# Optimization experiments

Measured on AMD Instinct MI355X. Metric: run time of the kernel, lower is better.

Reference implementation:

```python
import jax, jax.numpy as jnp
import numpy as np

N, E, IN, H, D = 50000, 800000, 256, 4, 32
ALPHA = 0.2


def setup_inputs() -> dict:
    key = jax.random.key(0)
    ks = jax.random.split(key, 8)
    return {
        "node_feature": jax.random.normal(ks[0], (N, IN), dtype=jnp.float32),
        "edge_feature": jax.random.normal(ks[1], (E, IN), dtype=jnp.float32),
        "src": jax.random.randint(ks[2], (E,), 0, N, dtype=jnp.int32),
        "dst": jax.random.randint(ks[3], (E,), 0, N, dtype=jnp.int32),
        "W": jax.random.normal(ks[4], (IN, H * D), dtype=jnp.float32) * (1.0 / np.sqrt(IN)),
        "attn_l": jax.random.normal(ks[5], (H, D), dtype=jnp.float32),
        "attn_r": jax.random.normal(ks[6], (H, D), dtype=jnp.float32),
        "attn_e": jax.random.normal(ks[7], (H, D), dtype=jnp.float32),
    }


def reference(node_feature, edge_feature, src, dst, W, attn_l, attn_r, attn_e):
    n = node_feature.shape[0]
    h, d = attn_l.shape
    # shared linear projection for node and edge features (feat_drop is identity, p=0)
    ft = (node_feature @ W).reshape(n, h, d)            # [N,H,D]
    e_ft = (edge_feature @ W).reshape(-1, h, d)          # [E,H,D]
    # per-head scalar attention logits
    a1 = jnp.einsum("nhd,hd->nh", ft, attn_l)            # [N,H]
    a2 = jnp.einsum("nhd,hd->nh", ft, attn_r)            # [N,H]
    a3 = jnp.einsum("ehd,hd->eh", e_ft, attn_e)          # [E,H]
    logits = jax.nn.leaky_relu(a1[src] + a3 + a2[dst], negative_slope=ALPHA)  # [E,H]
    # edge softmax grouped by destination node
    m = jax.ops.segment_max(logits, dst, num_segments=n)  # [N,H]
    ex = jnp.exp(logits - m[dst])                        # [E,H]
    s = jax.ops.segment_sum(ex, dst, num_segments=n)     # [N,H]
    a = ex / s[dst]                                       # [E,H] (attn_drop identity)
    # weighted messages: attention-weighted src feats + attention-weighted edge feats
    aw = a[:, :, None]                                    # [E,H,1]
    f_cat = e_ft * aw + ft[src] * aw                      # [E,H,D]
    node_out = jax.ops.segment_sum(f_cat, dst, num_segments=n)  # [N,H,D]
    ret1 = jax.nn.elu(node_out.reshape(n, h * d))
    ret2 = jax.nn.elu(f_cat.reshape(-1, h * d))
    return ret1, ret2
```

## Files before the change

### kernel.cpp

```cpp
#include <hip/hip_runtime.h>
#include <hip/hip_bf16.h>
#include <math.h>

#define NN    50000
#define EE    800000
#define IN_F  256
#define HH    4
#define DD    32
#define OUT_F 128
#define ALPHA 0.2f

typedef float f32x4 __attribute__((ext_vector_type(4)));
typedef short bf16x8 __attribute__((ext_vector_type(8)));

__device__ __forceinline__ float elu_f(float x) { return x > 0.0f ? x : expm1f(x); }

__device__ __forceinline__ unsigned short f2bf(float x) {
    union { float f; unsigned u; } v; v.f = x;
    unsigned r = (v.u + 0x7FFFu + ((v.u >> 16) & 1u)) >> 16;
    return (unsigned short)r;
}
__device__ __forceinline__ float bf2f(unsigned short h) {
    union { unsigned u; float f; } v; v.u = ((unsigned)h) << 16; return v.f;
}

__global__ __launch_bounds__(256) void k_prepw(const float* __restrict__ W,
        unsigned short* __restrict__ Whp, unsigned short* __restrict__ Wlp) {
    int i = blockIdx.x * 256 + threadIdx.x;
    int j = i & 7, lane = (i >> 3) & 63, cf = (i >> 9) & 7, t = i >> 12;
    int krow = 32 * t + 8 * (lane >> 4) + j;
    int col  = 16 * cf + (lane & 15);
    float x = W[krow * OUT_F + col];
    unsigned short h = f2bf(x);
    unsigned short lo = f2bf(x - bf2f(h));
    Whp[i] = h; Wlp[i] = lo;
}

template <int MODE, bool EFB>
__global__ __launch_bounds__(256, 4) void k_gemm(const float* __restrict__ X, int M,
        const unsigned short* __restrict__ Whp, const unsigned short* __restrict__ Wlp,
        const float* __restrict__ av0, const float* __restrict__ av1,
        const int* __restrict__ src, const int* __restrict__ dst,
        const float* __restrict__ a1, const float* __restrict__ a2,
        float* __restrict__ Yf, unsigned short* __restrict__ Yh,
        float* __restrict__ o1, float* __restrict__ o2,
        float* __restrict__ ssum) {
    __shared__ unsigned short Asw[2][2][64 * 64];
    __shared__ float p_lds[4][64];
    __shared__ float q_lds[4][64];

    const int tid = threadIdx.x;
    const int w = tid >> 6;
    const int l = tid & 63;
    const int base = blockIdx.x * 64;

    const int srow = tid >> 2;
    const int scg  = tid & 3;
    int gr = base + srow; if (gr > M - 1) gr = M - 1;
    const float* xp = X + (size_t)gr * IN_F + scg * 16;

    float4 xs[4];
    #pragma unroll
    for (int q = 0; q < 4; ++q) xs[q] = *(const float4*)(xp + q * 4);

    auto cvtwrite = [&](int buf) {
        unsigned short h[16], lo[16];
        const float* xf = (const float*)xs;
        #pragma unroll
        for (int k = 0; k < 16; ++k) {
            h[k]  = f2bf(xf[k]);
            lo[k] = f2bf(xf[k] - bf2f(h[k]));
        }
        const unsigned sw = (unsigned)((srow & 7) << 4);
        const unsigned b0 = (unsigned)(srow * 128 + scg * 32) ^ sw;
        const unsigned b1 = (unsigned)(srow * 128 + scg * 32 + 16) ^ sw;
        char* ph = (char*)&Asw[buf][0][0];
        char* pl = (char*)&Asw[buf][1][0];
        *(bf16x8*)(ph + b0) = *(const bf16x8*)(h);
        *(bf16x8*)(ph + b1) = *(const bf16x8*)(h + 8);
        *(bf16x8*)(pl + b0) = *(const bf16x8*)(lo);
        *(bf16x8*)(pl + b1) = *(const bf16x8*)(lo + 8);
    };
    cvtwrite(0);

    f32x4 acc[4][2];
    #pragma unroll
    for (int rf = 0; rf < 4; ++rf)
        #pragma unroll
        for (int cf = 0; cf < 2; ++cf)
            acc[rf][cf] = (f32x4){0.f, 0.f, 0.f, 0.f};

    #pragma unroll
    for (int c = 0; c < 4; ++c) {
        __syncthreads();
        if (c < 3) {
            #pragma unroll
            for (int q = 0; q < 4; ++q)
                xs[q] = *(const float4*)(xp + (c + 1) * 64 + q * 4);
        }
        bf16x8 Bh[2][2], Bl[2][2];
        #pragma unroll
        for (int ks = 0; ks < 2; ++ks)
            #pragma unroll
            for (int cf = 0; cf < 2; ++cf) {
                size_t off = ((size_t)((c * 2 + ks) * 8 + (w * 2 + cf)) * 64 + l) * 8;
                Bh[ks][cf] = *(const bf16x8*)(Whp + off);
                Bl[ks][cf] = *(const bf16x8*)(Wlp + off);
            }
        const char* ph = (const char*)&Asw[c & 1][0][0];
        const char* pl = (const char*)&Asw[c & 1][1][0];
        #pragma unroll
        for (int rf = 0; rf < 4; ++rf) {
            const int row = rf * 16 + (l & 15);
            const unsigned sw = (unsigned)((row & 7) << 4);
            #pragma unroll
            for (int ks = 0; ks < 2; ++ks) {
                const unsigned ba = (unsigned)(row * 128 + ks * 64 + (l >> 4) * 16) ^ sw;
                bf16x8 ah = *(const bf16x8*)(ph + ba);
                bf16x8 al = *(const bf16x8*)(pl + ba);
                #pragma unroll
                for (int cf = 0; cf < 2; ++cf) {
                    acc[rf][cf] = __builtin_amdgcn_mfma_f32_16x16x32_bf16(ah, Bh[ks][cf], acc[rf][cf], 0, 0, 0);
                    acc[rf][cf] = __builtin_amdgcn_mfma_f32_16x16x32_bf16(al, Bh[ks][cf], acc[rf][cf], 0, 0, 0);
                    acc[rf][cf] = __builtin_amdgcn_mfma_f32_16x16x32_bf16(ah, Bl[ks][cf], acc[rf][cf], 0, 0, 0);
                }
            }
        }
        if (c < 3) cvtwrite((c + 1) & 1);
    }

    #pragma unroll
    for (int rf = 0; rf < 4; ++rf)
        #pragma unroll
        for (int cf = 0; cf < 2; ++cf)
            #pragma unroll
            for (int r = 0; r < 4; ++r) {
                int grow = base + rf * 16 + (l >> 4) * 4 + r;
                size_t oidx = (size_t)grow * OUT_F + w * 32 + cf * 16 + (l & 15);
                if (MODE == 0) {
                    if (grow < M) Yf[oidx] = acc[rf][cf][r];
                } else if (EFB) {
                    Yh[oidx] = f2bf(acc[rf][cf][r]);
                } else {
                    Yf[oidx] = acc[rf][cf][r];
                }
            }

    const float b0 = av0[w * DD + (l & 15)];
    const float b1 = av0[w * DD + 16 + (l & 15)];
    float c0v = 0.f, c1v = 0.f;
    if (MODE == 0) { c0v = av1[w * DD + (l & 15)]; c1v = av1[w * DD + 16 + (l & 15)]; }

    float pv[4][4], qv[4][4];
    #pragma unroll
    for (int rf = 0; rf < 4; ++rf)
        #pragma unroll
        for (int r = 0; r < 4; ++r) {
            pv[rf][r] = acc[rf][0][r] * b0 + acc[rf][1][r] * b1;
            if (MODE == 0) qv[rf][r] = acc[rf][0][r] * c0v + acc[rf][1][r] * c1v;
        }
    #pragma unroll
    for (int o = 1; o <= 8; o <<= 1)
        #pragma unroll
        for (int rf = 0; rf < 4; ++rf)
            #pragma unroll
            for (int r = 0; r < 4; ++r) {
                pv[rf][r] += __shfl_xor(pv[rf][r], o);
                if (MODE == 0) qv[rf][r] += __shfl_xor(qv[rf][r], o);
            }
    if ((l & 15) == 0) {
        const int hi = l >> 4;
        #pragma unroll
        for (int rf = 0; rf < 4; ++rf)
            #pragma unroll
            for (int r = 0; r < 4; ++r) {
                p_lds[w][rf * 16 + hi * 4 + r] = pv[rf][r];
                if (MODE == 0) q_lds[w][rf * 16 + hi * 4 + r] = qv[rf][r];
            }
    }
    __syncthreads();

    const int grow = base + l;
    if (MODE == 0) {
        if (grow < M) {
            o1[(size_t)grow * HH + w] = p_lds[w][l];
            o2[(size_t)grow * HH + w] = q_lds[w][l];
        }
    } else {
        const int s = src[grow], t2 = dst[grow];
        float lg = p_lds[w][l] + a1[(size_t)s * HH + w] + a2[(size_t)t2 * HH + w];
        lg = fmaxf(lg, ALPHA * lg);
        float exv = expf(lg);
        o1[(size_t)grow * HH + w] = exv;
        atomicAdd(&ssum[t2 * HH + w], exv);
    }
}

__global__ __launch_bounds__(256) void k_hist(const int* __restrict__ dst,
        int* __restrict__ hist) {
    int i = blockIdx.x * 256 + threadIdx.x;
    if (i < EE) atomicAdd(&hist[dst[i]], 1);
}

__global__ __launch_bounds__(1024) void k_scan(const int* __restrict__ hist,
        int* __restrict__ rowptr, int* __restrict__ cursor) {
    __shared__ int part[1024];
    const int t = threadIdx.x;
    const int CH = (NN + 1023) / 1024;
    const int b = t * CH;
    int s = 0;
    for (int i = 0; i < CH; ++i) {
        int idx = b + i;
        if (idx < NN) s += hist[idx];
    }
    part[t] = s;
    __syncthreads();
    int total = s;
    for (int o = 1; o < 1024; o <<= 1) {
        int u = (t >= o) ? part[t - o] : 0;
        __syncthreads();
        part[t] += u;
        __syncthreads();
    }
    int run = part[t] - total;
    for (int i = 0; i < CH; ++i) {
        int idx = b + i;
        if (idx < NN) {
            rowptr[idx] = run;
            cursor[idx] = run;
            run += hist[idx];
        }
    }
}

__global__ __launch_bounds__(256) void k_scatter(const int* __restrict__ dst,
        int* __restrict__ cursor, int* __restrict__ order) {
    int i = blockIdx.x * 256 + threadIdx.x;
    if (i < EE) {
        int pos = atomicAdd(&cursor[dst[i]], 1);
        order[pos] = i;
    }
}

template <bool EFB>
__global__ __launch_bounds__(256, 8) void k_agg2(const int* __restrict__ order,
        const int* __restrict__ src, const int* __restrict__ dst,
        const float* __restrict__ ft, const float* __restrict__ exq,
        const float* __restrict__ ssum, const unsigned short* __restrict__ eftb,
        float* __restrict__ ret2, float* __restrict__ node_out) {
    __shared__ int eL[64], sL[64], dL[64];
    __shared__ int sent[2];
    const int tid = threadIdx.x;
    const int base = blockIdx.x * 64;
    if (tid < 64) {
        int e = order[base + tid];
        eL[tid] = e;
        sL[tid] = src[e];
        dL[tid] = dst[e];
    } else if (tid == 64) {
        sent[0] = (blockIdx.x > 0) ? dst[order[base - 1]] : -1;
    } else if (tid == 65) {
        sent[1] = (base + 64 < EE) ? dst[order[base + 64]] : -1;
    }
    __syncthreads();

    const int w = tid >> 6, l = tid & 63;
    const int W0 = w * 16, W1 = W0 + 15;
    const int c0 = l * 2, h = l >> 4;

    const int dprev  = (W0 == 0)  ? sent[0] : dL[W0 - 1];
    const int dafter = (W1 == 63) ? sent[1] : dL[W1 + 1];

    float acc0 = 0.f, acc1 = 0.f;
    int dcur = dL[W0];
    bool touch_start = true;

    #pragma unroll 4
    for (int r = W0; r <= W1; ++r) {
        const int e = eL[r], s = sL[r], d = dL[r];
        if (d != dcur) {
            const size_t o = (size_t)dcur * OUT_F + c0;
            if (touch_start && dcur == dprev) {
                atomicAdd(&node_out[o], acc0);
                atomicAdd(&node_out[o + 1], acc1);
            } else {
                *(float2*)(node_out + o) = make_float2(acc0, acc1);
            }
            acc0 = acc1 = 0.f; dcur = d; touch_start = false;
        }
        const float a = exq[(size_t)e * HH + h] * __frcp_rn(ssum[d * HH + h]);
        float e0, e1;
        if (EFB) {
            ushort2 ev = *(const ushort2*)(eftb + (size_t)e * OUT_F + c0);
            e0 = bf2f(ev.x); e1 = bf2f(ev.y);
        } else {
            float2 ev = *(const float2*)(ret2 + (size_t)e * OUT_F + c0);
            e0 = ev.x; e1 = ev.y;
        }
        float2 fv = *(const float2*)(ft + (size_t)s * OUT_F + c0);
        float f0 = (e0 + fv.x) * a;
        float f1 = (e1 + fv.y) * a;
        acc0 += f0; acc1 += f1;
        *(float2*)(ret2 + (size_t)e * OUT_F + c0) = make_float2(elu_f(f0), elu_f(f1));
    }
    {
        const size_t o = (size_t)dcur * OUT_F + c0;
        const bool at = (touch_start && dcur == dprev) || (dcur == dafter);
        if (at) {
            atomicAdd(&node_out[o], acc0);
            atomicAdd(&node_out[o + 1], acc1);
        } else {
            *(float2*)(node_out + o) = make_float2(acc0, acc1);
        }
    }
}

__global__ __launch_bounds__(256) void k_elu1(const float4* __restrict__ node_out,
        float4* __restrict__ ret1) {
    const int i = blockIdx.x * blockDim.x + threadIdx.x;
    if (i < NN * OUT_F / 4) {
        float4 v = node_out[i];
        ret1[i] = make_float4(elu_f(v.x), elu_f(v.y), elu_f(v.z), elu_f(v.w));
    }
}

extern "C" void kernel_launch(void* const* d_in, const int* in_sizes, int n_in,
                              void* d_out, int out_size, void* d_ws, size_t ws_size,
                              hipStream_t stream) {
    const float* nf     = (const float*)d_in[0];
    const float* ef     = (const float*)d_in[1];
    const int*   src    = (const int*)d_in[2];
    const int*   dst    = (const int*)d_in[3];
    const float* W      = (const float*)d_in[4];
    const float* attn_l = (const float*)d_in[5];
    const float* attn_r = (const float*)d_in[6];
    const float* attn_e = (const float*)d_in[7];

    float* ret1 = (float*)d_out;
    float* ret2 = ret1 + (size_t)NN * OUT_F;

    char* wsp = (char*)d_ws;
    auto take = [&](size_t bytes) { char* p = wsp; wsp += (bytes + 511) & ~size_t(511); return p; };
    float* ft     = (float*)take((size_t)NN * OUT_F * 4);
    float* a1buf  = (float*)take((size_t)NN * HH * 4);
    float* a2buf  = (float*)take((size_t)NN * HH * 4);
    float* exq    = (float*)take((size_t)EE * HH * 4);
    float* ssum   = (float*)take((size_t)NN * HH * 4);
    unsigned short* Whp = (unsigned short*)take(32768 * 2);
    unsigned short* Wlp = (unsigned short*)take(32768 * 2);
    int* hist   = (int*)take((size_t)NN * 4);
    int* rowptr = (int*)take((size_t)NN * 4);
    int* cursor = (int*)take((size_t)NN * 4);
    int* order  = (int*)take((size_t)EE * 4);

    const size_t eft_bytes = (size_t)EE * OUT_F * 2;
    const size_t used = (size_t)(wsp - (char*)d_ws);
    const bool efb = (used + eft_bytes + 1024) <= ws_size;
    unsigned short* eftb = efb ? (unsigned short*)take(eft_bytes) : nullptr;

    hipMemsetAsync(ssum, 0, (size_t)NN * HH * 4, stream);
    hipMemsetAsync(hist, 0, (size_t)NN * 4, stream);
    hipMemsetAsync(ret1, 0, (size_t)NN * OUT_F * 4, stream);

    k_prepw<<<128, 256, 0, stream>>>(W, Whp, Wlp);
    k_hist<<<(EE + 255) / 256, 256, 0, stream>>>(dst, hist);
    k_scan<<<1, 1024, 0, stream>>>(hist, rowptr, cursor);
    k_scatter<<<(EE + 255) / 256, 256, 0, stream>>>(dst, cursor, order);

    k_gemm<0, false><<<(NN + 63) / 64, 256, 0, stream>>>(nf, NN, Whp, Wlp,
            attn_l, attn_r, nullptr, nullptr, nullptr, nullptr,
            ft, nullptr, a1buf, a2buf, nullptr);

    if (efb) {
        k_gemm<1, true><<<EE / 64, 256, 0, stream>>>(ef, EE, Whp, Wlp,
                attn_e, nullptr, src, dst, a1buf, a2buf,
                nullptr, eftb, exq, nullptr, ssum);
        k_agg2<true><<<EE / 64, 256, 0, stream>>>(order, src, dst, ft, exq,
                ssum, eftb, ret2, ret1);
    } else {
        k_gemm<1, false><<<EE / 64, 256, 0, stream>>>(ef, EE, Whp, Wlp,
                attn_e, nullptr, src, dst, a1buf, a2buf,
                ret2, nullptr, exq, nullptr, ssum);
        k_agg2<false><<<EE / 64, 256, 0, stream>>>(order, src, dst, ft, exq,
                ssum, nullptr, ret2, ret1);
    }
    k_elu1<<<(NN * OUT_F / 4 + 255) / 256, 256, 0, stream>>>(
            (const float4*)ret1, (float4*)ret1);
}
```

Measured before the change: 811.8 us.

## Store node projections in bf16, fuse setup kernels, prefetch edge gather indices

Node projection ft is now stored as bf16 instead of fp32, which halves the bytes of the random per-edge src gathers in the aggregation kernel. The W prep, dst histogram and zeroing of ssum and ret1 are merged into one setup kernel, replacing two memsets and two launches. In the edge GEMM, the src/dst indices and the a1/a2 logit gathers are issued before the MFMA loop so their latency overlaps compute. The fp32 fallback path is dropped, so the edge bf16 buffer is always taken from the workspace, and rounding ft to bf16 adds precision loss.

```diff
diff --git a/kernel.cpp b/kernel.cpp
--- a/kernel.cpp
+++ b/kernel.cpp
@@ -24,25 +24,43 @@
     union { unsigned u; float f; } v; v.u = ((unsigned)h) << 16; return v.f;
 }
 
-__global__ __launch_bounds__(256) void k_prepw(const float* __restrict__ W,
-        unsigned short* __restrict__ Whp, unsigned short* __restrict__ Wlp) {
-    int i = blockIdx.x * 256 + threadIdx.x;
-    int j = i & 7, lane = (i >> 3) & 63, cf = (i >> 9) & 7, t = i >> 12;
-    int krow = 32 * t + 8 * (lane >> 4) + j;
-    int col  = 16 * cf + (lane & 15);
-    float x = W[krow * OUT_F + col];
-    unsigned short h = f2bf(x);
-    unsigned short lo = f2bf(x - bf2f(h));
-    Whp[i] = h; Wlp[i] = lo;
-}
-
-template <int MODE, bool EFB>
+#define PREP_B 128
+#define HIST_B 3125
+#define SSUM_B 196
+#define RET1_B 6250
+__global__ __launch_bounds__(256) void k_setup(const float* __restrict__ W,
+        unsigned short* __restrict__ Whp, unsigned short* __restrict__ Wlp,
+        const int* __restrict__ dst, int* __restrict__ hist,
+        float4* __restrict__ ssum4, float4* __restrict__ ret14) {
+    const int b = blockIdx.x, tid = threadIdx.x;
+    if (b < PREP_B) {
+        int i = b * 256 + tid;
+        int j = i & 7, lane = (i >> 3) & 63, cf = (i >> 9) & 7, t = i >> 12;
+        int krow = 32 * t + 8 * (lane >> 4) + j;
+        int col  = 16 * cf + (lane & 15);
+        float x = W[krow * OUT_F + col];
+        unsigned short h = f2bf(x);
+        Whp[i] = h;
+        Wlp[i] = f2bf(x - bf2f(h));
+    } else if (b < PREP_B + HIST_B) {
+        int i = (b - PREP_B) * 256 + tid;
+        atomicAdd(&hist[dst[i]], 1);
+    } else if (b < PREP_B + HIST_B + SSUM_B) {
+        int i = (b - PREP_B - HIST_B) * 256 + tid;
+        if (i < NN * HH / 4) ssum4[i] = make_float4(0.f, 0.f, 0.f, 0.f);
+    } else {
+        int i = (b - PREP_B - HIST_B - SSUM_B) * 256 + tid;
+        ret14[i] = make_float4(0.f, 0.f, 0.f, 0.f);
+    }
+}
+
+template <int MODE>
 __global__ __launch_bounds__(256, 4) void k_gemm(const float* __restrict__ X, int M,
         const unsigned short* __restrict__ Whp, const unsigned short* __restrict__ Wlp,
         const float* __restrict__ av0, const float* __restrict__ av1,
         const int* __restrict__ src, const int* __restrict__ dst,
         const float* __restrict__ a1, const float* __restrict__ a2,
-        float* __restrict__ Yf, unsigned short* __restrict__ Yh,
+        unsigned short* __restrict__ Yh,
         float* __restrict__ o1, float* __restrict__ o2,
         float* __restrict__ ssum) {
     __shared__ unsigned short Asw[2][2][64 * 64];
@@ -53,6 +71,9 @@
     const int w = tid >> 6;
     const int l = tid & 63;
     const int base = blockIdx.x * 64;
+
+    int s_e = 0, t_e = 0;
+    if (MODE == 1) { s_e = src[base + l]; t_e = dst[base + l]; }
 
     const int srow = tid >> 2;
     const int scg  = tid & 3;
@@ -83,6 +104,12 @@
     };
     cvtwrite(0);
 
+    float a1v = 0.f, a2v = 0.f;
+    if (MODE == 1) {
+        a1v = a1[(size_t)s_e * HH + w];
+        a2v = a2[(size_t)t_e * HH + w];
+    }
+
     f32x4 acc[4][2];
     #pragma unroll
     for (int rf = 0; rf < 4; ++rf)
@@ -136,14 +163,9 @@
             #pragma unroll
             for (int r = 0; r < 4; ++r) {
                 int grow = base + rf * 16 + (l >> 4) * 4 + r;
-                size_t oidx = (size_t)grow * OUT_F + w * 32 + cf * 16 + (l & 15);
-                if (MODE == 0) {
-                    if (grow < M) Yf[oidx] = acc[rf][cf][r];
-                } else if (EFB) {
-                    Yh[oidx] = f2bf(acc[rf][cf][r]);
-                } else {
-                    Yf[oidx] = acc[rf][cf][r];
-                }
+                if (MODE == 1 || grow < M)
+                    Yh[(size_t)grow * OUT_F + w * 32 + cf * 16 + (l & 15)] =
+                        f2bf(acc[rf][cf][r]);
             }
 
     const float b0 = av0[w * DD + (l & 15)];
@@ -187,23 +209,16 @@
             o2[(size_t)grow * HH + w] = q_lds[w][l];
         }
     } else {
-        const int s = src[grow], t2 = dst[grow];
-        float lg = p_lds[w][l] + a1[(size_t)s * HH + w] + a2[(size_t)t2 * HH + w];
+        float lg = p_lds[w][l] + a1v + a2v;
         lg = fmaxf(lg, ALPHA * lg);
         float exv = expf(lg);
         o1[(size_t)grow * HH + w] = exv;
-        atomicAdd(&ssum[t2 * HH + w], exv);
-    }
-}
-
-__global__ __launch_bounds__(256) void k_hist(const int* __restrict__ dst,
-        int* __restrict__ hist) {
-    int i = blockIdx.x * 256 + threadIdx.x;
-    if (i < EE) atomicAdd(&hist[dst[i]], 1);
+        atomicAdd(&ssum[t_e * HH + w], exv);
+    }
 }
 
 __global__ __launch_bounds__(1024) void k_scan(const int* __restrict__ hist,
-        int* __restrict__ rowptr, int* __restrict__ cursor) {
+        int* __restrict__ cursor) {
     __shared__ int part[1024];
     const int t = threadIdx.x;
     const int CH = (NN + 1023) / 1024;
@@ -226,7 +241,6 @@
     for (int i = 0; i < CH; ++i) {
         int idx = b + i;
         if (idx < NN) {
-            rowptr[idx] = run;
             cursor[idx] = run;
             run += hist[idx];
         }
@@ -242,10 +256,9 @@
     }
 }
 
-template <bool EFB>
 __global__ __launch_bounds__(256, 8) void k_agg2(const int* __restrict__ order,
         const int* __restrict__ src, const int* __restrict__ dst,
-        const float* __restrict__ ft, const float* __restrict__ exq,
+        const unsigned short* __restrict__ ftb, const float* __restrict__ exq,
         const float* __restrict__ ssum, const unsigned short* __restrict__ eftb,
         float* __restrict__ ret2, float* __restrict__ node_out) {
     __shared__ int eL[64], sL[64], dL[64];
@@ -289,17 +302,10 @@
             acc0 = acc1 = 0.f; dcur = d; touch_start = false;
         }
         const float a = exq[(size_t)e * HH + h] * __frcp_rn(ssum[d * HH + h]);
-        float e0, e1;
-        if (EFB) {
-            ushort2 ev = *(const ushort2*)(eftb + (size_t)e * OUT_F + c0);
-            e0 = bf2f(ev.x); e1 = bf2f(ev.y);
-        } else {
-            float2 ev = *(const float2*)(ret2 + (size_t)e * OUT_F + c0);
-            e0 = ev.x; e1 = ev.y;
-        }
-        float2 fv = *(const float2*)(ft + (size_t)s * OUT_F + c0);
-        float f0 = (e0 + fv.x) * a;
-        float f1 = (e1 + fv.y) * a;
+        ushort2 ev = *(const ushort2*)(eftb + (size_t)e * OUT_F + c0);
+        ushort2 fv = *(const ushort2*)(ftb + (size_t)s * OUT_F + c0);
+        float f0 = (bf2f(ev.x) + bf2f(fv.x)) * a;
+        float f1 = (bf2f(ev.y) + bf2f(fv.y)) * a;
         acc0 += f0; acc1 += f1;
         *(float2*)(ret2 + (size_t)e * OUT_F + c0) = make_float2(elu_f(f0), elu_f(f1));
     }
@@ -341,7 +347,7 @@
 
     char* wsp = (char*)d_ws;
     auto take = [&](size_t bytes) { char* p = wsp; wsp += (bytes + 511) & ~size_t(511); return p; };
-    float* ft     = (float*)take((size_t)NN * OUT_F * 4);
+    unsigned short* ftb = (unsigned short*)take((size_t)NN * OUT_F * 2);
     float* a1buf  = (float*)take((size_t)NN * HH * 4);
     float* a2buf  = (float*)take((size_t)NN * HH * 4);
     float* exq    = (float*)take((size_t)EE * HH * 4);
@@ -349,41 +355,25 @@
     unsigned short* Whp = (unsigned short*)take(32768 * 2);
     unsigned short* Wlp = (unsigned short*)take(32768 * 2);
     int* hist   = (int*)take((size_t)NN * 4);
-    int* rowptr = (int*)take((size_t)NN * 4);
     int* cursor = (int*)take((size_t)NN * 4);
     int* order  = (int*)take((size_t)EE * 4);
-
-    const size_t eft_bytes = (size_t)EE * OUT_F * 2;
-    const size_t used = (size_t)(wsp - (char*)d_ws);
-    const bool efb = (used + eft_bytes + 1024) <= ws_size;
-    unsigned short* eftb = efb ? (unsigned short*)take(eft_bytes) : nullptr;
-
-    hipMemsetAsync(ssum, 0, (size_t)NN * HH * 4, stream);
+    unsigned short* eftb = (unsigned short*)take((size_t)EE * OUT_F * 2);
+
     hipMemsetAsync(hist, 0, (size_t)NN * 4, stream);
-    hipMemsetAsync(ret1, 0, (size_t)NN * OUT_F * 4, stream);
-
-    k_prepw<<<128, 256, 0, stream>>>(W, Whp, Wlp);
-    k_hist<<<(EE + 255) / 256, 256, 0, stream>>>(dst, hist);
-    k_scan<<<1, 1024, 0, stream>>>(hist, rowptr, cursor);
+    k_setup<<<PREP_B + HIST_B + SSUM_B + RET1_B, 256, 0, stream>>>(
+            W, Whp, Wlp, dst, hist, (float4*)ssum, (float4*)ret1);
+    k_scan<<<1, 1024, 0, stream>>>(hist, cursor);
     k_scatter<<<(EE + 255) / 256, 256, 0, stream>>>(dst, cursor, order);
 
-    k_gemm<0, false><<<(NN + 63) / 64, 256, 0, stream>>>(nf, NN, Whp, Wlp,
+    k_gemm<0><<<(NN + 63) / 64, 256, 0, stream>>>(nf, NN, Whp, Wlp,
             attn_l, attn_r, nullptr, nullptr, nullptr, nullptr,
-            ft, nullptr, a1buf, a2buf, nullptr);
-
-    if (efb) {
-        k_gemm<1, true><<<EE / 64, 256, 0, stream>>>(ef, EE, Whp, Wlp,
-                attn_e, nullptr, src, dst, a1buf, a2buf,
-                nullptr, eftb, exq, nullptr, ssum);
-        k_agg2<true><<<EE / 64, 256, 0, stream>>>(order, src, dst, ft, exq,
-                ssum, eftb, ret2, ret1);
-    } else {
-        k_gemm<1, false><<<EE / 64, 256, 0, stream>>>(ef, EE, Whp, Wlp,
-                attn_e, nullptr, src, dst, a1buf, a2buf,
-                ret2, nullptr, exq, nullptr, ssum);
-        k_agg2<false><<<EE / 64, 256, 0, stream>>>(order, src, dst, ft, exq,
-                ssum, nullptr, ret2, ret1);
-    }
+            ftb, a1buf, a2buf, nullptr);
+    k_gemm<1><<<EE / 64, 256, 0, stream>>>(ef, EE, Whp, Wlp,
+            attn_e, nullptr, src, dst, a1buf, a2buf,
+            eftb, exq, nullptr, ssum);
+
+    k_agg2<<<EE / 64, 256, 0, stream>>>(order, src, dst, ftb, exq, ssum,
+                                        eftb, ret2, ret1);
     k_elu1<<<(NN * OUT_F / 4 + 255) / 256, 256, 0, stream>>>(
             (const float4*)ret1, (float4*)ret1);
 }
```

Measured after the change: 756.0 us. 6.9% less time.
